# Optimization experiments

Hardware: AMD Instinct MI355X
Metric: run time of the kernel (lower is better)

## Reference

```python
import jax, jax.numpy as jnp
jax.config.update("jax_enable_x64", True)
import numpy as np


def _quat_to_rot(q):
    q = q / jnp.linalg.norm(q)
    a, b, c, d = q[0], q[1], q[2], q[3]
    return jnp.stack([
        1 - 2 * c * c - 2 * d * d, 2 * b * c - 2 * a * d, 2 * a * c + 2 * b * d,
        2 * b * c + 2 * a * d, 1 - 2 * b * b - 2 * d * d, 2 * c * d - 2 * a * b,
        2 * b * d - 2 * a * c, 2 * a * b + 2 * c * d, 1 - 2 * b * b - 2 * c * c,
    ]).reshape(3, 3)


def _chamfer(x, y):
    # x: [N,4], y: [M,4]; fp64 cdist + bidirectional min-reduction (memory-bound)
    x = x.astype(jnp.float64)
    y = y.astype(jnp.float64)
    d2 = (jnp.sum(x * x, -1)[:, None] + jnp.sum(y * y, -1)[None, :]
          - 2.0 * x @ y.T)
    d = jnp.sqrt(jnp.maximum(d2, 0.0))
    return jnp.min(d, axis=1).mean() + jnp.min(d, axis=0).mean()


def _revolute_transform(anchor, axis, theta):
    # anchor: [3] (a,b,c), axis: [3] (u,v,w), theta scalar -> 4x4 screw rotation
    a, b, c = anchor[0], anchor[1], anchor[2]
    u, v, w = axis[0], axis[1], axis[2]
    cos = jnp.cos(theta)
    sin = jnp.sin(theta)
    top = jnp.stack([
        u * u + (v * v + w * w) * cos, u * v * (1 - cos) - w * sin, u * w * (1 - cos) + v * sin,
        (a * (v * v + w * w) - u * (b * v + c * w)) * (1 - cos) + (b * w - c * v) * sin,
        u * v * (1 - cos) + w * sin, v * v + (u * u + w * w) * cos, v * w * (1 - cos) - u * sin,
        (b * (u * u + w * w) - v * (a * u + c * w)) * (1 - cos) + (c * u - a * w) * sin,
        u * w * (1 - cos) - v * sin, v * w * (1 - cos) + u * sin, w * w + (u * u + v * v) * cos,
        (c * (u * u + v * v) - w * (a * u + b * v)) * (1 - cos) + (a * v - b * u) * sin,
    ]).reshape(3, 4)
    bottom = jnp.array([[0.0, 0.0, 0.0, 1.0]], dtype=top.dtype)
    return jnp.concatenate([top, bottom], axis=0)


def setup_inputs() -> dict:
    key = jax.random.key(0)
    ks = jax.random.split(key, 8)
    P, N = 2, 8192
    return {
        "camera_pts": jax.random.normal(ks[0], (P, N, 3), dtype=jnp.float32),
        "cad_pts": jax.random.normal(ks[1], (P, N, 3), dtype=jnp.float32),
        "xyz": jax.random.normal(ks[2], (P - 1, 3), dtype=jnp.float32),
        "rpy": jax.random.normal(ks[3], (P - 1, 3), dtype=jnp.float32),
        "part_weight": jax.random.uniform(ks[4], (P,), dtype=jnp.float32),
        "base_r_quat": jax.random.normal(ks[5], (4,), dtype=jnp.float32),
        "base_t": jax.random.normal(ks[6], (3, 1), dtype=jnp.float32),
        "joint_state": jax.random.normal(ks[7], (P - 1,), dtype=jnp.float32),
    }


def reference(camera_pts, cad_pts, xyz, rpy, part_weight, base_r_quat, base_t, joint_state):
    num_parts = camera_pts.shape[0]
    num_joints = num_parts - 1
    ones = jnp.ones(camera_pts.shape[:-1] + (1,), dtype=camera_pts.dtype)
    cam_h = jnp.concatenate([camera_pts, ones], axis=-1)  # [P,N,4]
    cad_h = jnp.concatenate([cad_pts, ones], axis=-1)     # [P,N,4]

    base_rot = _quat_to_rot(base_r_quat)
    base_transform = jnp.concatenate([
        jnp.concatenate([base_rot, base_t], axis=1),
        jnp.array([[0.0, 0.0, 0.0, 1.0]], dtype=base_rot.dtype),
    ], axis=0)  # 4x4

    cad_base = cad_h[0] @ base_transform.T
    base_objective = _chamfer(cad_base, cam_h[0])
    all_objective = part_weight[0] * base_objective

    child_objectives = []
    rel_transforms = []
    for j in range(num_joints):
        rel = _revolute_transform(xyz[j], rpy[j], joint_state[j])
        rel_transforms.append(rel)
        T = rel @ base_transform
        cad_child = cad_h[j + 1] @ T.T
        obj = _chamfer(cad_child, cam_h[j + 1])
        child_objectives.append(obj)
        all_objective = all_objective + part_weight[j + 1] * obj

    all_objective = all_objective / num_parts
    relative_transform_all = jnp.stack(rel_transforms, axis=0)
    child_objective_all = jnp.stack(child_objectives, axis=0)
    return (all_objective, base_objective, child_objective_all,
            base_transform, relative_transform_all)
```

## Files before the change

kernel.cpp:

```cpp
#include <hip/hip_runtime.h>
#include <math.h>

#define NPTS 8192

struct Xforms { float B[3][4]; float R[3][4]; float T[3][4]; };

__device__ __forceinline__ void compute_xforms(const float* __restrict__ quat,
                                               const float* __restrict__ bt,
                                               const float* __restrict__ anchor,
                                               const float* __restrict__ axis,
                                               const float* __restrict__ theta,
                                               Xforms& X) {
  float q0 = quat[0], q1 = quat[1], q2 = quat[2], q3 = quat[3];
  float n = sqrtf(q0 * q0 + q1 * q1 + q2 * q2 + q3 * q3);
  float a = q0 / n, b = q1 / n, c = q2 / n, d = q3 / n;
  X.B[0][0] = 1.f - 2.f * c * c - 2.f * d * d;
  X.B[0][1] = 2.f * b * c - 2.f * a * d;
  X.B[0][2] = 2.f * a * c + 2.f * b * d;
  X.B[0][3] = bt[0];
  X.B[1][0] = 2.f * b * c + 2.f * a * d;
  X.B[1][1] = 1.f - 2.f * b * b - 2.f * d * d;
  X.B[1][2] = 2.f * c * d - 2.f * a * b;
  X.B[1][3] = bt[1];
  X.B[2][0] = 2.f * b * d - 2.f * a * c;
  X.B[2][1] = 2.f * a * b + 2.f * c * d;
  X.B[2][2] = 1.f - 2.f * b * b - 2.f * c * c;
  X.B[2][3] = bt[2];

  float ax = anchor[0], ay = anchor[1], az = anchor[2];
  float u = axis[0], v = axis[1], w = axis[2];
  float th = theta[0];
  float cs = cosf(th), sn = sinf(th), oc = 1.f - cs;
  X.R[0][0] = u * u + (v * v + w * w) * cs;
  X.R[0][1] = u * v * oc - w * sn;
  X.R[0][2] = u * w * oc + v * sn;
  X.R[0][3] = (ax * (v * v + w * w) - u * (ay * v + az * w)) * oc + (ay * w - az * v) * sn;
  X.R[1][0] = u * v * oc + w * sn;
  X.R[1][1] = v * v + (u * u + w * w) * cs;
  X.R[1][2] = v * w * oc - u * sn;
  X.R[1][3] = (ay * (u * u + w * w) - v * (ax * u + az * w)) * oc + (az * u - ax * w) * sn;
  X.R[2][0] = u * w * oc - v * sn;
  X.R[2][1] = v * w * oc + u * sn;
  X.R[2][2] = w * w + (u * u + v * v) * cs;
  X.R[2][3] = (az * (u * u + v * v) - w * (ax * u + ay * v)) * oc + (ax * v - ay * u) * sn;

#pragma unroll
  for (int i = 0; i < 3; i++) {
#pragma unroll
    for (int j = 0; j < 4; j++) {
      float s = X.R[i][0] * X.B[0][j] + X.R[i][1] * X.B[1][j] + X.R[i][2] * X.B[2][j];
      if (j == 3) s += X.R[i][3];
      X.T[i][j] = s;
    }
  }
}

__global__ __launch_bounds__(256) void prep_kernel(
    const float* __restrict__ cam, const float* __restrict__ cad,
    const float* __restrict__ quat, const float* __restrict__ bt,
    const float* __restrict__ anchor, const float* __restrict__ axis,
    const float* __restrict__ theta,
    float4* __restrict__ pts4, unsigned int* __restrict__ minarr,
    float* __restrict__ sums, unsigned int* __restrict__ counter) {
  int gid = blockIdx.x * 256 + threadIdx.x;
  minarr[gid] = 0x7f800000u;
  if (gid < 4) sums[gid] = 0.f;
  if (gid == 0) *counter = 0u;

  Xforms X;
  compute_xforms(quat, bt, anchor, axis, theta, X);

  int a = gid >> 13;
  int i = gid & 8191;
  int part = a >> 1;
  const float* base = ((a & 1) ? cam : cad) + part * NPTS * 3;
  float px = base[i * 3 + 0], py = base[i * 3 + 1], pz = base[i * 3 + 2];
  if ((a & 1) == 0) {
    float M[3][4];
#pragma unroll
    for (int r = 0; r < 3; r++)
#pragma unroll
      for (int cc = 0; cc < 4; cc++) M[r][cc] = part ? X.T[r][cc] : X.B[r][cc];
    float qx = M[0][0] * px + M[0][1] * py + M[0][2] * pz + M[0][3];
    float qy = M[1][0] * px + M[1][1] * py + M[1][2] * pz + M[1][3];
    float qz = M[2][0] * px + M[2][1] * py + M[2][2] * pz + M[2][3];
    px = qx; py = qy; pz = qz;
  }
  float h = 0.5f * (px * px + py * py + pz * pz);
  pts4[gid] = make_float4(px, py, pz, h);
}

__global__ __launch_bounds__(256) void chamfer_kernel(
    const float4* __restrict__ pts4, unsigned int* __restrict__ minarr) {
  const int combo = blockIdx.z;
  const int tid = threadIdx.x;
  const float4* __restrict__ srcp = pts4 + combo * NPTS;
  const float4* __restrict__ tgtp = pts4 + (combo ^ 1) * NPTS;

  const int sbase = blockIdx.x * 2048;

  float4 s[8];
  float vmin[8];
#pragma unroll
  for (int i = 0; i < 8; i++) {
    s[i] = srcp[sbase + i * 256 + tid];
    vmin[i] = 3.4e38f;
  }

  __shared__ float4 tile[256];
  tile[tid] = tgtp[blockIdx.y * 256 + tid];
  __syncthreads();

#pragma unroll 4
  for (int k = 0; k < 256; k++) {
    float4 t = tile[k];
#pragma unroll
    for (int i = 0; i < 8; i++) {
      float v = fmaf(-s[i].z, t.z, t.w);
      v = fmaf(-s[i].y, t.y, v);
      v = fmaf(-s[i].x, t.x, v);
      vmin[i] = fminf(vmin[i], v);
    }
  }

#pragma unroll
  for (int i = 0; i < 8; i++) {
    float d2 = fmaxf(0.f, 2.f * (s[i].w + vmin[i]));
    atomicMin(minarr + combo * NPTS + sbase + i * 256 + tid, __float_as_uint(d2));
  }
}

__global__ __launch_bounds__(256) void reduce_finalize_kernel(
    const unsigned int* __restrict__ minarr, float* __restrict__ sums,
    unsigned int* __restrict__ counter,
    const float* __restrict__ pw,
    const float* __restrict__ quat, const float* __restrict__ bt,
    const float* __restrict__ anchor, const float* __restrict__ axis,
    const float* __restrict__ theta, float* __restrict__ out) {
  const int tid = threadIdx.x;
  const int combo = blockIdx.x >> 3;
  const int chunk = blockIdx.x & 7;
  const int base = combo * NPTS + chunk * 1024;

  float ssum = 0.f;
#pragma unroll
  for (int j = 0; j < 4; j++)
    ssum += sqrtf(__uint_as_float(minarr[base + j * 256 + tid]));

#pragma unroll
  for (int off = 32; off > 0; off >>= 1) ssum += __shfl_down(ssum, off);
  __shared__ float part[4];
  if ((tid & 63) == 0) part[tid >> 6] = ssum;
  __syncthreads();

  if (tid == 0) {
    float blocksum = part[0] + part[1] + part[2] + part[3];
    atomicAdd(&sums[combo], blocksum);
    __threadfence();
    unsigned int old = atomicAdd(counter, 1u);
    if (old == 31u) {
      __threadfence();
      float s0 = __hip_atomic_load(&sums[0], __ATOMIC_ACQUIRE, __HIP_MEMORY_SCOPE_AGENT);
      float s1 = __hip_atomic_load(&sums[1], __ATOMIC_ACQUIRE, __HIP_MEMORY_SCOPE_AGENT);
      float s2 = __hip_atomic_load(&sums[2], __ATOMIC_ACQUIRE, __HIP_MEMORY_SCOPE_AGENT);
      float s3 = __hip_atomic_load(&sums[3], __ATOMIC_ACQUIRE, __HIP_MEMORY_SCOPE_AGENT);
      Xforms X;
      compute_xforms(quat, bt, anchor, axis, theta, X);
      const float inv = 1.0f / (float)NPTS;
      float base_obj = (s0 + s1) * inv;
      float child_obj = (s2 + s3) * inv;
      out[0] = (pw[0] * base_obj + pw[1] * child_obj) * 0.5f;
      out[1] = base_obj;
      out[2] = child_obj;
      for (int i = 0; i < 3; i++)
        for (int j = 0; j < 4; j++) out[3 + i * 4 + j] = X.B[i][j];
      out[15] = 0.f; out[16] = 0.f; out[17] = 0.f; out[18] = 1.f;
      for (int i = 0; i < 3; i++)
        for (int j = 0; j < 4; j++) out[19 + i * 4 + j] = X.R[i][j];
      out[31] = 0.f; out[32] = 0.f; out[33] = 0.f; out[34] = 1.f;
    }
  }
}

extern "C" void kernel_launch(void* const* d_in, const int* in_sizes, int n_in,
                              void* d_out, int out_size, void* d_ws, size_t ws_size,
                              hipStream_t stream) {
  const float* cam  = (const float*)d_in[0];
  const float* cad  = (const float*)d_in[1];
  const float* xyz  = (const float*)d_in[2];
  const float* rpy  = (const float*)d_in[3];
  const float* pw   = (const float*)d_in[4];
  const float* quat = (const float*)d_in[5];
  const float* bt   = (const float*)d_in[6];
  const float* js   = (const float*)d_in[7];

  unsigned int* minarr = (unsigned int*)d_ws;
  float4* pts4 = (float4*)((char*)d_ws + 4 * NPTS * sizeof(unsigned int));
  float* sums = (float*)((char*)d_ws + 4 * NPTS * sizeof(unsigned int) + 4 * NPTS * sizeof(float4));
  unsigned int* counter = (unsigned int*)(sums + 4);
  float* out = (float*)d_out;

  hipLaunchKernelGGL(prep_kernel, dim3(128), dim3(256), 0, stream,
                     cam, cad, quat, bt, xyz, rpy, js, pts4, minarr, sums, counter);
  hipLaunchKernelGGL(chamfer_kernel, dim3(4, 32, 4), dim3(256), 0, stream,
                     pts4, minarr);
  hipLaunchKernelGGL(reduce_finalize_kernel, dim3(32), dim3(256), 0, stream,
                     minarr, sums, counter, pw, quat, bt, xyz, rpy, js, out);
}
```

Measured before the change: 100.7 us.

## Fuse point transform into chamfer kernel and replace atomicMin with partial-min buffer

Drops the separate prep kernel: each chamfer block now loads raw points, applies the rigid transform and norm term inline, and recomputes the transforms itself. Per-point atomicMin is replaced by plain stores into a per-target-tile partial minimum buffer (64 tiles of 128 targets), which a wider reduce kernel min-reduces before summing. This removes one launch and the atomic contention, at the cost of redundant transform work, a larger workspace (8 MB of partials), and extra reduce-kernel memory traffic.

```diff
diff --git a/kernel.cpp b/kernel.cpp
--- a/kernel.cpp
+++ b/kernel.cpp
@@ -2,6 +2,11 @@
 #include <math.h>
 
 #define NPTS 8192
+#define TCH 64
+#define TILE 128
+#define SCH 4
+#define SPB 2048
+#define NRED 128
 
 struct Xforms { float B[3][4]; float R[3][4]; float T[3][4]; };
 
@@ -55,64 +60,71 @@
   }
 }
 
-__global__ __launch_bounds__(256) void prep_kernel(
+__global__ __launch_bounds__(256, 4) void chamfer_kernel(
     const float* __restrict__ cam, const float* __restrict__ cad,
     const float* __restrict__ quat, const float* __restrict__ bt,
     const float* __restrict__ anchor, const float* __restrict__ axis,
     const float* __restrict__ theta,
-    float4* __restrict__ pts4, unsigned int* __restrict__ minarr,
-    float* __restrict__ sums, unsigned int* __restrict__ counter) {
-  int gid = blockIdx.x * 256 + threadIdx.x;
-  minarr[gid] = 0x7f800000u;
-  if (gid < 4) sums[gid] = 0.f;
-  if (gid == 0) *counter = 0u;
+    float* __restrict__ minpart, float* __restrict__ sums,
+    unsigned int* __restrict__ counter) {
+  const int tid = threadIdx.x;
+  if (blockIdx.x == 0 && blockIdx.y == 0 && blockIdx.z == 0) {
+    if (tid < 4) sums[tid] = 0.f;
+    if (tid == 4) *counter = 0u;
+  }
 
   Xforms X;
   compute_xforms(quat, bt, anchor, axis, theta, X);
 
-  int a = gid >> 13;
-  int i = gid & 8191;
-  int part = a >> 1;
-  const float* base = ((a & 1) ? cam : cad) + part * NPTS * 3;
-  float px = base[i * 3 + 0], py = base[i * 3 + 1], pz = base[i * 3 + 2];
-  if ((a & 1) == 0) {
-    float M[3][4];
-#pragma unroll
-    for (int r = 0; r < 3; r++)
-#pragma unroll
-      for (int cc = 0; cc < 4; cc++) M[r][cc] = part ? X.T[r][cc] : X.B[r][cc];
-    float qx = M[0][0] * px + M[0][1] * py + M[0][2] * pz + M[0][3];
-    float qy = M[1][0] * px + M[1][1] * py + M[1][2] * pz + M[1][3];
-    float qz = M[2][0] * px + M[2][1] * py + M[2][2] * pz + M[2][3];
-    px = qx; py = qy; pz = qz;
-  }
-  float h = 0.5f * (px * px + py * py + pz * pz);
-  pts4[gid] = make_float4(px, py, pz, h);
-}
-
-__global__ __launch_bounds__(256) void chamfer_kernel(
-    const float4* __restrict__ pts4, unsigned int* __restrict__ minarr) {
   const int combo = blockIdx.z;
-  const int tid = threadIdx.x;
-  const float4* __restrict__ srcp = pts4 + combo * NPTS;
-  const float4* __restrict__ tgtp = pts4 + (combo ^ 1) * NPTS;
-
-  const int sbase = blockIdx.x * 2048;
+  const int part = combo >> 1;
+  const int dir = combo & 1;
+
+  float M[3][4];
+#pragma unroll
+  for (int i = 0; i < 3; i++)
+#pragma unroll
+    for (int j = 0; j < 4; j++) M[i][j] = part ? X.T[i][j] : X.B[i][j];
+
+  const float* __restrict__ srcraw = (dir ? cam : cad) + part * NPTS * 3;
+  const float* __restrict__ tgtraw = (dir ? cad : cam) + part * NPTS * 3;
+  const bool src_xf = (dir == 0);
+  const bool tgt_xf = (dir == 1);
+
+  const int sbase = blockIdx.x * SPB;
 
   float4 s[8];
   float vmin[8];
 #pragma unroll
   for (int i = 0; i < 8; i++) {
-    s[i] = srcp[sbase + i * 256 + tid];
+    int idx = sbase + i * 256 + tid;
+    float px = srcraw[idx * 3 + 0], py = srcraw[idx * 3 + 1], pz = srcraw[idx * 3 + 2];
+    if (src_xf) {
+      float qx = M[0][0] * px + M[0][1] * py + M[0][2] * pz + M[0][3];
+      float qy = M[1][0] * px + M[1][1] * py + M[1][2] * pz + M[1][3];
+      float qz = M[2][0] * px + M[2][1] * py + M[2][2] * pz + M[2][3];
+      px = qx; py = qy; pz = qz;
+    }
+    s[i] = make_float4(px, py, pz, 0.5f * (px * px + py * py + pz * pz));
     vmin[i] = 3.4e38f;
   }
 
-  __shared__ float4 tile[256];
-  tile[tid] = tgtp[blockIdx.y * 256 + tid];
+  __shared__ float4 tile[TILE];
+  if (tid < TILE) {
+    int idx = blockIdx.y * TILE + tid;
+    float px = tgtraw[idx * 3 + 0], py = tgtraw[idx * 3 + 1], pz = tgtraw[idx * 3 + 2];
+    if (tgt_xf) {
+      float qx = M[0][0] * px + M[0][1] * py + M[0][2] * pz + M[0][3];
+      float qy = M[1][0] * px + M[1][1] * py + M[1][2] * pz + M[1][3];
+      float qz = M[2][0] * px + M[2][1] * py + M[2][2] * pz + M[2][3];
+      px = qx; py = qy; pz = qz;
+    }
+    tile[tid] = make_float4(px, py, pz, 0.5f * (px * px + py * py + pz * pz));
+  }
   __syncthreads();
 
 #pragma unroll 4
-  for (int k = 0; k < 256; k++) {
+  for (int k = 0; k < TILE; k++) {
     float4 t = tile[k];
 #pragma unroll
     for (int i = 0; i < 8; i++) {
@@ -123,29 +135,34 @@
     }
   }
 
+  float* __restrict__ slot = minpart + ((combo * TCH + blockIdx.y) << 13) + sbase;
 #pragma unroll
   for (int i = 0; i < 8; i++) {
-    float d2 = fmaxf(0.f, 2.f * (s[i].w + vmin[i]));
-    atomicMin(minarr + combo * NPTS + sbase + i * 256 + tid, __float_as_uint(d2));
+    slot[i * 256 + tid] = fmaxf(0.f, 2.f * (s[i].w + vmin[i]));
   }
 }
 
 __global__ __launch_bounds__(256) void reduce_finalize_kernel(
-    const unsigned int* __restrict__ minarr, float* __restrict__ sums,
+    const float* __restrict__ minpart, float* __restrict__ sums,
     unsigned int* __restrict__ counter,
     const float* __restrict__ pw,
     const float* __restrict__ quat, const float* __restrict__ bt,
     const float* __restrict__ anchor, const float* __restrict__ axis,
     const float* __restrict__ theta, float* __restrict__ out) {
   const int tid = threadIdx.x;
-  const int combo = blockIdx.x >> 3;
-  const int chunk = blockIdx.x & 7;
-  const int base = combo * NPTS + chunk * 1024;
-
-  float ssum = 0.f;
-#pragma unroll
-  for (int j = 0; j < 4; j++)
-    ssum += sqrtf(__uint_as_float(minarr[base + j * 256 + tid]));
+  const int combo = blockIdx.x >> 5;
+  const int pt = (blockIdx.x & 31) * 256 + tid;
+  const float* __restrict__ mp = minpart + combo * TCH * NPTS + pt;
+
+  float m0 = 3.4e38f, m1 = 3.4e38f, m2 = 3.4e38f, m3 = 3.4e38f;
+#pragma unroll
+  for (int c = 0; c < TCH; c += 4) {
+    m0 = fminf(m0, mp[(c + 0) * NPTS]);
+    m1 = fminf(m1, mp[(c + 1) * NPTS]);
+    m2 = fminf(m2, mp[(c + 2) * NPTS]);
+    m3 = fminf(m3, mp[(c + 3) * NPTS]);
+  }
+  float ssum = sqrtf(fminf(fminf(m0, m1), fminf(m2, m3)));
 
 #pragma unroll
   for (int off = 32; off > 0; off >>= 1) ssum += __shfl_down(ssum, off);
@@ -158,7 +175,7 @@
     atomicAdd(&sums[combo], blocksum);
     __threadfence();
     unsigned int old = atomicAdd(counter, 1u);
-    if (old == 31u) {
+    if (old == NRED - 1) {
       __threadfence();
       float s0 = __hip_atomic_load(&sums[0], __ATOMIC_ACQUIRE, __HIP_MEMORY_SCOPE_AGENT);
       float s1 = __hip_atomic_load(&sums[1], __ATOMIC_ACQUIRE, __HIP_MEMORY_SCOPE_AGENT);
@@ -194,16 +211,13 @@
   const float* bt   = (const float*)d_in[6];
   const float* js   = (const float*)d_in[7];
 
-  unsigned int* minarr = (unsigned int*)d_ws;
-  float4* pts4 = (float4*)((char*)d_ws + 4 * NPTS * sizeof(unsigned int));
-  float* sums = (float*)((char*)d_ws + 4 * NPTS * sizeof(unsigned int) + 4 * NPTS * sizeof(float4));
+  float* minpart = (float*)d_ws;
+  float* sums = (float*)((char*)d_ws + (size_t)4 * TCH * NPTS * sizeof(float));
   unsigned int* counter = (unsigned int*)(sums + 4);
   float* out = (float*)d_out;
 
-  hipLaunchKernelGGL(prep_kernel, dim3(128), dim3(256), 0, stream,
-                     cam, cad, quat, bt, xyz, rpy, js, pts4, minarr, sums, counter);
-  hipLaunchKernelGGL(chamfer_kernel, dim3(4, 32, 4), dim3(256), 0, stream,
-                     pts4, minarr);
-  hipLaunchKernelGGL(reduce_finalize_kernel, dim3(32), dim3(256), 0, stream,
-                     minarr, sums, counter, pw, quat, bt, xyz, rpy, js, out);
-}
+  hipLaunchKernelGGL(chamfer_kernel, dim3(SCH, TCH, 4), dim3(256), 0, stream,
+                     cam, cad, quat, bt, xyz, rpy, js, minpart, sums, counter);
+  hipLaunchKernelGGL(reduce_finalize_kernel, dim3(NRED), dim3(256), 0, stream,
+                     minpart, sums, counter, pw, quat, bt, xyz, rpy, js, out);
+}
```

Result: no change. 101.7 us (+1.0%).
